# Kernel optimization log

Measured on AMD Instinct MI355X. Metric: run time of the kernel, lower is better.

The kernel has to match this reference:

```python
import jax, jax.numpy as jnp
import numpy as np

B, N, E = 4, 4096, 16384
D, A_DIM = 256, 64
T, HALF, STEPS, NTYPES = 16, 8, 3, 50


def setup_inputs() -> dict:
    key = jax.random.key(0)
    ks = jax.random.split(key, 16)
    s = 0.02  # small init so repeated DxD matmuls stay stable over 3 steps
    return {
        "annotation_id": jax.random.randint(ks[0], (B, N), 0, NTYPES),
        "src": jax.random.randint(ks[1], (B, E), 0, N),
        "dst": jax.random.randint(ks[2], (B, E), 0, N),
        "etype": jax.random.randint(ks[3], (B, E), 0, HALF),
        "edge_embed": jax.random.normal(ks[4], (T, D * D), jnp.float32) * s,
        "edge_bias": jax.random.normal(ks[5], (T, D), jnp.float32) * s,
        "type_embed": jax.random.normal(ks[6], (NTYPES, A_DIM), jnp.float32) * s,
        "Wr": jax.random.normal(ks[7], (D, 3 * D), jnp.float32) * s,
        "br": jnp.zeros((D,), jnp.float32),
        "Wz": jax.random.normal(ks[8], (D, 3 * D), jnp.float32) * s,
        "bz": jnp.zeros((D,), jnp.float32),
        "Wh": jax.random.normal(ks[9], (D, 3 * D), jnp.float32) * s,
        "bh": jnp.zeros((D,), jnp.float32),
        "Wa": jax.random.normal(ks[10], (1, D + A_DIM), jnp.float32) * s,
        "ba": jnp.zeros((1,), jnp.float32),
        "Wo": jax.random.normal(ks[11], (1, D + A_DIM), jnp.float32) * s,
        "bo": jnp.zeros((1,), jnp.float32),
    }


def reference(annotation_id, src, dst, etype, edge_embed, edge_bias, type_embed,
              Wr, br, Wz, bz, Wh, bh, Wa, ba, Wo, bo):
    # annotation: typeEmbed[id-1] if id>0 else zeros  -> [B, N, A_DIM]
    ann = jnp.where((annotation_id > 0)[..., None],
                    type_embed[jnp.clip(annotation_id - 1, 0, NTYPES - 1)],
                    jnp.zeros((), type_embed.dtype))
    # prop_state: annotation zero-padded to state_dim  -> [B, N, D]
    h = jnp.concatenate([ann, jnp.zeros((B, N, D - A_DIM), ann.dtype)], axis=-1)
    W = edge_embed.reshape(T, D, D)  # per-edge-type DxD matrices

    def step(h):
        # type-major projection: apply every edge-type matrix to every node state
        # P[b, t, n, :] = W[t] @ h[b, n]   -> [B, T, N, D]
        P = jnp.einsum('tij,bnj->btni', W, h)

        def per_graph(Pg, s_, d_, e_):
            # a_out[j]        += W[e] @ h[neighbour] + b[e]
            # a_in[neighbour] += W[e+HALF] @ h[j]   + b[e+HALF]
            m_out = Pg[e_, d_] + edge_bias[e_]            # [E, D]
            m_in = Pg[e_ + HALF, s_] + edge_bias[e_ + HALF]
            a_out = jnp.zeros((N, D), h.dtype).at[s_].add(m_out)
            a_in = jnp.zeros((N, D), h.dtype).at[d_].add(m_in)
            return a_in, a_out

        a_in, a_out = jax.vmap(per_graph)(P, src, dst, etype)
        # GRU-style propagator (dropout_rate = 0 -> identity)
        a = jnp.concatenate([a_in, a_out, h], axis=-1)    # [B, N, 3D]
        r = jax.nn.sigmoid(a @ Wr.T + br)
        z = jax.nn.sigmoid(a @ Wz.T + bz)
        h_hat = jnp.tanh(jnp.concatenate([a_in, a_out, r * h], axis=-1) @ Wh.T + bh)
        return (1.0 - z) * h + z * h_hat

    for _ in range(STEPS):
        h = step(h)

    join = jnp.concatenate([h, ann], axis=-1)             # [B, N, D+A]
    atten = jax.nn.sigmoid(join @ Wa.T + ba)              # [B, N, 1]
    ou = jnp.tanh(join @ Wo.T + bo)                       # [B, N, 1]
    w_sum = jnp.sum((atten * ou).reshape(-1, N), axis=1)  # [B]
    return jax.nn.sigmoid(w_sum)
```

## Files before the change

kernel.cpp:

```cpp
#include <hip/hip_runtime.h>
#include <cstdint>

#define BB 4
#define NN 4096
#define EE 16384
#define DD 256
#define ADIM 64
#define TT 16
#define HALFE 8
#define STEPS 3
#define OSTRIDE 4160
#define MAXTILES 1088
#define MAXM (MAXTILES * 128)

#define AS1 __attribute__((address_space(1)))
#define AS3 __attribute__((address_space(3)))

typedef __attribute__((ext_vector_type(8))) short short8;
typedef __attribute__((ext_vector_type(4))) float f32x4;

__device__ __forceinline__ float sigmoidf_(float x) { return 1.0f / (1.0f + __expf(-x)); }

__device__ __forceinline__ unsigned short f2bf(float x) {
    unsigned u = __float_as_uint(x);
    u += 0x7fffu + ((u >> 16) & 1u);
    return (unsigned short)(u >> 16);
}
__device__ __forceinline__ float bf2f(unsigned short b) {
    return __uint_as_float(((unsigned)b) << 16);
}

__global__ void init_kernel(const int* __restrict__ ann_id,
                            const float* __restrict__ type_embed,
                            float* __restrict__ ann, float* __restrict__ h,
                            unsigned short* __restrict__ hbf,
                            unsigned short* __restrict__ Xbf) {
    int idx = blockIdx.x * 256 + threadIdx.x;
    int bn = idx >> 6, q = idx & 63;
    int id = ann_id[bn];
    float4 v = {0.f, 0.f, 0.f, 0.f};
    if (q < 16) {
        if (id > 0) v = ((const float4*)(type_embed + (size_t)(id - 1) * ADIM))[q];
        ((float4*)(ann + (size_t)bn * ADIM))[q] = v;
    }
    ((float4*)(h + (size_t)bn * DD))[q] = v;
    ushort4 o;
    o.x = f2bf(v.x); o.y = f2bf(v.y); o.z = f2bf(v.z); o.w = f2bf(v.w);
    ((ushort4*)(hbf + (size_t)bn * DD))[q] = o;
    ((ushort4*)(Xbf + (size_t)bn * 768 + 512))[q] = o;
}

__global__ void conv_f2b4(const float* __restrict__ in, unsigned short* __restrict__ out) {
    int idx = blockIdx.x * 256 + threadIdx.x;
    float4 v = ((const float4*)in)[idx];
    ushort4 o;
    o.x = f2bf(v.x); o.y = f2bf(v.y); o.z = f2bf(v.z); o.w = f2bf(v.w);
    ((ushort4*)out)[idx] = o;
}

__global__ void build_wcat(const float* __restrict__ Wr, const float* __restrict__ Wz,
                           const float* __restrict__ Wh, unsigned short* __restrict__ W) {
    int idx = blockIdx.x * 256 + threadIdx.x;
    int c = idx / 768, k = idx % 768;
    float v;
    if (c < 256)       v = Wr[c * 768 + k];
    else if (c < 512)  v = Wz[(c - 256) * 768 + k];
    else               v = (k < 512) ? Wh[(c - 512) * 768 + k] : 0.f;
    W[idx] = f2bf(v);
}

__global__ void build_whh(const float* __restrict__ Wh, unsigned short* __restrict__ W) {
    int idx = blockIdx.x * 256 + threadIdx.x;
    int i = idx / 256, k = idx % 256;
    W[idx] = f2bf(Wh[i * 768 + 512 + k]);
}

__global__ void count_kernel(const int* __restrict__ src, const int* __restrict__ dst,
                             int* __restrict__ counts) {
    int idx = blockIdx.x * 256 + threadIdx.x;
    int b = idx >> 14;
    atomicAdd(&counts[(b * 2 + 0) * NN + src[idx]], 1);
    atomicAdd(&counts[(b * 2 + 1) * NN + dst[idx]], 1);
}

__global__ __launch_bounds__(1024) void scan_kernel(const int* __restrict__ counts,
                                                    int* __restrict__ offs,
                                                    int* __restrict__ cursor) {
    __shared__ int lsum[1024];
    int t = threadIdx.x, seg = blockIdx.x;
    int4 v = ((const int4*)(counts + (size_t)seg * NN))[t];
    int s1 = v.x + v.y, s2 = s1 + v.z, s3 = s2 + v.w;
    lsum[t] = s3;
    __syncthreads();
    for (int off = 1; off < 1024; off <<= 1) {
        int tmp = (t >= off) ? lsum[t - off] : 0;
        __syncthreads();
        lsum[t] += tmp;
        __syncthreads();
    }
    int base = lsum[t] - s3;
    int* o = offs + (size_t)seg * OSTRIDE;
    o[4 * t] = base; o[4 * t + 1] = base + v.x; o[4 * t + 2] = base + s1; o[4 * t + 3] = base + s2;
    if (t == 1023) o[4096] = lsum[1023];
    int* c = cursor + (size_t)seg * NN;
    c[4 * t] = base; c[4 * t + 1] = base + v.x; c[4 * t + 2] = base + s1; c[4 * t + 3] = base + s2;
}

__global__ void count2_kernel(const int* __restrict__ et, int* __restrict__ c32) {
    __shared__ int cnt[32];
    int tid = threadIdx.x;
    if (tid < 32) cnt[tid] = 0;
    __syncthreads();
    int idx = blockIdx.x * 256 + tid;
    int b = idx >> 14;
    atomicAdd(&cnt[b * 8 + et[idx]], 1);
    __syncthreads();
    if (tid < 32) atomicAdd(&c32[tid], cnt[tid]);
}

__global__ void scan2_kernel(const int* __restrict__ c32, int* __restrict__ type_cursor,
                             int* __restrict__ tile_type) {
    __shared__ int pad[64];
    int t = threadIdx.x;
    int b = t >> 4, dir = (t >> 3) & 1, tt = t & 7;
    int cnt = c32[b * 8 + tt];
    int padded = ((cnt + 127) >> 7) << 7;
    pad[t] = padded;
    __syncthreads();
    int off = 0;
    for (int k = 0; k < t; ++k) off += pad[k];
    type_cursor[t] = off;
    int t16 = dir * 8 + tt;
    int tile0 = off >> 7;
    for (int k = 0; k < (padded >> 7); ++k) tile_type[tile0 + k] = t16;
}

__global__ void fill2_kernel(const int* __restrict__ src, const int* __restrict__ dst,
                             const int* __restrict__ et, int* __restrict__ type_cursor,
                             int* __restrict__ node_cursor, int* __restrict__ entries,
                             int* __restrict__ idx2) {
    __shared__ int cnt[64];
    __shared__ int bse[64];
    int tid = threadIdx.x;
    if (tid < 64) cnt[tid] = 0;
    __syncthreads();
    int idx = blockIdx.x * 256 + tid;
    int b = idx >> 14;
    int s = src[idx], d = dst[idx], t = et[idx];
    int bin0 = b * 16 + t;
    int bin1 = b * 16 + 8 + t;
    int r0 = atomicAdd(&cnt[bin0], 1);
    int r1 = atomicAdd(&cnt[bin1], 1);
    __syncthreads();
    if (tid < 64) bse[tid] = atomicAdd(&type_cursor[tid], cnt[tid]);
    __syncthreads();
    int p0 = bse[bin0] + r0;
    int p1 = bse[bin1] + r1;
    idx2[p0] = b * NN + d;
    idx2[p1] = b * NN + s;
    int q0 = atomicAdd(&node_cursor[(b * 2 + 0) * NN + s], 1);
    entries[(size_t)(b * 2 + 0) * EE + q0] = (p0 << 4) | t;
    int q1 = atomicAdd(&node_cursor[(b * 2 + 1) * NN + d], 1);
    entries[(size_t)(b * 2 + 1) * EE + q1] = (p1 << 4) | (t + 8);
}


#define GEMM_CORE_128x64(A_, Bt_, K_)                                                   \
    const int tid = threadIdx.x;                                                        \
    const int wv = tid >> 6, lane = tid & 63;                                           \
    const int wr = wv >> 1, wc = wv & 1;                                                \
    const int lr = lane & 15, hi = lane >> 4, rx = lane & 7;                            \
    const int srow = wv * 8 + (lane >> 3);                                              \
    const int scol = ((lane & 7) ^ (lane >> 3)) << 3;                                   \
    const unsigned short* Ag = A_ + (size_t)(r0 + srow) * K_ + scol;                    \
    const unsigned short* Bg = Bt_ + (size_t)(c0 + srow) * K_ + scol;                   \
    f32x4 acc[4][2] = {};                                                               \
    for (int k0 = 0; k0 < K_; k0 += 64) {                                               \
        _Pragma("unroll")                                                               \
        for (int i = 0; i < 4; ++i)                                                     \
            __builtin_amdgcn_global_load_lds(                                           \
                (const AS1 void*)(Ag + (size_t)(i * 32) * K_ + k0),                     \
                (AS3 void*)((char*)As + wv * 1024 + i * 4096), 16, 0, 0);               \
        _Pragma("unroll")                                                               \
        for (int i = 0; i < 2; ++i)                                                     \
            __builtin_amdgcn_global_load_lds(                                           \
                (const AS1 void*)(Bg + (size_t)(i * 32) * K_ + k0),                     \
                (AS3 void*)((char*)Bs + wv * 1024 + i * 4096), 16, 0, 0);               \
        __syncthreads();                                                                \
        _Pragma("unroll")                                                               \
        for (int kk = 0; kk < 2; ++kk) {                                                \
            short8 af[4], bfv[2];                                                       \
            _Pragma("unroll")                                                           \
            for (int m = 0; m < 4; ++m) {                                               \
                int R = wr * 64 + m * 16 + lr;                                          \
                af[m] = *(const short8*)((const char*)As + R * 128 + (((kk * 4 + hi) ^ rx) << 4)); \
            }                                                                           \
            _Pragma("unroll")                                                           \
            for (int n = 0; n < 2; ++n) {                                               \
                int R = wc * 32 + n * 16 + lr;                                          \
                bfv[n] = *(const short8*)((const char*)Bs + R * 128 + (((kk * 4 + hi) ^ rx) << 4)); \
            }                                                                           \
            _Pragma("unroll")                                                           \
            for (int m = 0; m < 4; ++m)                                                 \
                _Pragma("unroll")                                                       \
                for (int n = 0; n < 2; ++n)                                             \
                    acc[m][n] = __builtin_amdgcn_mfma_f32_16x16x32_bf16(bfv[n], af[m], acc[m][n], 0, 0, 0); \
        }                                                                               \
        __syncthreads();                                                                \
    }                                                                                   \
    const int erow = r0 + wr * 64 + lr;                                                 \
    const int ecol = c0 + wc * 32 + (hi << 2);

__global__ __launch_bounds__(256) void gemm_msgs(const unsigned short* __restrict__ A,
                                                 const unsigned short* __restrict__ W2,
                                                 const int* __restrict__ idx2,
                                                 const int* __restrict__ tile_type,
                                                 unsigned short* __restrict__ C) {
    __shared__ __align__(16) unsigned short As[128 * 64];
    __shared__ __align__(16) unsigned short Bs[64 * 64];
    const int bid = blockIdx.x;
    const int wg = (bid & 7) * (MAXTILES * 4 / 8) + (bid >> 3);
    const int by = wg >> 2, bx = wg & 3;
    const int t16 = tile_type[by];
    if (t16 < 0) return;
    const int r0 = by << 7, c0 = bx << 6;
    const int tid = threadIdx.x;
    const int wv = tid >> 6, lane = tid & 63;
    const int wr = wv >> 1, wc = wv & 1;
    const int lr = lane & 15, hi = lane >> 4, rx = lane & 7;
    const int srow = wv * 8 + (lane >> 3);
    const int scol = ((lane & 7) ^ (lane >> 3)) << 3;
    int ar[4];
#pragma unroll
    for (int i = 0; i < 4; ++i) ar[i] = idx2[r0 + srow + i * 32];
    const unsigned short* Bg = W2 + (size_t)t16 * (DD * DD) + (size_t)(c0 + srow) * DD + scol;
    f32x4 acc[4][2] = {};
    for (int k0 = 0; k0 < DD; k0 += 64) {
#pragma unroll
        for (int i = 0; i < 4; ++i)
            __builtin_amdgcn_global_load_lds(
                (const AS1 void*)(A + (size_t)ar[i] * DD + scol + k0),
                (AS3 void*)((char*)As + wv * 1024 + i * 4096), 16, 0, 0);
#pragma unroll
        for (int i = 0; i < 2; ++i)
            __builtin_amdgcn_global_load_lds(
                (const AS1 void*)(Bg + (size_t)(i * 32) * DD + k0),
                (AS3 void*)((char*)Bs + wv * 1024 + i * 4096), 16, 0, 0);
        __syncthreads();
#pragma unroll
        for (int kk = 0; kk < 2; ++kk) {
            short8 af[4], bfv[2];
#pragma unroll
            for (int m = 0; m < 4; ++m) {
                int R = wr * 64 + m * 16 + lr;
                af[m] = *(const short8*)((const char*)As + R * 128 + (((kk * 4 + hi) ^ rx) << 4));
            }
#pragma unroll
            for (int n = 0; n < 2; ++n) {
                int R = wc * 32 + n * 16 + lr;
                bfv[n] = *(const short8*)((const char*)Bs + R * 128 + (((kk * 4 + hi) ^ rx) << 4));
            }
#pragma unroll
            for (int m = 0; m < 4; ++m)
#pragma unroll
                for (int n = 0; n < 2; ++n)
                    acc[m][n] = __builtin_amdgcn_mfma_f32_16x16x32_bf16(bfv[n], af[m], acc[m][n], 0, 0, 0);
        }
        __syncthreads();
    }
    const int erow = r0 + wr * 64 + lr;
    const int ecol = c0 + wc * 32 + (hi << 2);
#pragma unroll
    for (int m = 0; m < 4; ++m)
#pragma unroll
        for (int n = 0; n < 2; ++n) {
            ushort4 o;
            o.x = f2bf(acc[m][n][0]); o.y = f2bf(acc[m][n][1]);
            o.z = f2bf(acc[m][n][2]); o.w = f2bf(acc[m][n][3]);
            *(ushort4*)&C[(size_t)(erow + m * 16) * DD + ecol + n * 16] = o;
        }
}

__global__ __launch_bounds__(256) void gemm_rzu(const unsigned short* __restrict__ A,
                                                const unsigned short* __restrict__ Bt,
                                                const float* __restrict__ br,
                                                const float* __restrict__ bz,
                                                const float* __restrict__ h,
                                                unsigned short* __restrict__ RH,
                                                unsigned short* __restrict__ Zb,
                                                unsigned short* __restrict__ Ub) {
    __shared__ __align__(16) unsigned short As[128 * 64];
    __shared__ __align__(16) unsigned short Bs[64 * 64];
    const int bid = blockIdx.x;
    const int wg = (bid & 7) * 192 + (bid >> 3);
    const int bx = wg % 12, by = wg / 12;
    const int r0 = by << 7, c0 = bx << 6;
    GEMM_CORE_128x64(A, Bt, 768)
    const int region = c0 >> 8;
#pragma unroll
    for (int m = 0; m < 4; ++m)
#pragma unroll
        for (int n = 0; n < 2; ++n) {
            int gr = erow + m * 16;
            int gc = ecol + n * 16;
            f32x4 v = acc[m][n];
            if (region == 0) {
                float4 bb = *(const float4*)&br[gc];
                float4 hv = *(const float4*)&h[(size_t)gr * 256 + gc];
                ushort4 o;
                o.x = f2bf(sigmoidf_(v[0] + bb.x) * hv.x);
                o.y = f2bf(sigmoidf_(v[1] + bb.y) * hv.y);
                o.z = f2bf(sigmoidf_(v[2] + bb.z) * hv.z);
                o.w = f2bf(sigmoidf_(v[3] + bb.w) * hv.w);
                *(ushort4*)&RH[(size_t)gr * 256 + gc] = o;
            } else if (region == 1) {
                int c = gc - 256;
                float4 bb = *(const float4*)&bz[c];
                ushort4 o;
                o.x = f2bf(sigmoidf_(v[0] + bb.x));
                o.y = f2bf(sigmoidf_(v[1] + bb.y));
                o.z = f2bf(sigmoidf_(v[2] + bb.z));
                o.w = f2bf(sigmoidf_(v[3] + bb.w));
                *(ushort4*)&Zb[(size_t)gr * 256 + c] = o;
            } else {
                int c = gc - 512;
                ushort4 o;
                o.x = f2bf(v[0]); o.y = f2bf(v[1]); o.z = f2bf(v[2]); o.w = f2bf(v[3]);
                *(ushort4*)&Ub[(size_t)gr * 256 + c] = o;
            }
        }
}

__global__ __launch_bounds__(256) void gemm_hh(const unsigned short* __restrict__ A,
                                               const unsigned short* __restrict__ Bt,
                                               const unsigned short* __restrict__ Zb,
                                               const unsigned short* __restrict__ Ub,
                                               const float* __restrict__ bh,
                                               float* __restrict__ h,
                                               unsigned short* __restrict__ hbf,
                                               unsigned short* __restrict__ Xbf) {
    __shared__ __align__(16) unsigned short As[64 * 64];
    __shared__ __align__(16) unsigned short Bs[64 * 64];
    const int bid = blockIdx.x;
    const int wg = (bid & 7) * 128 + (bid >> 3);
    const int by = wg >> 2, bx = wg & 3;
    const int r0 = by << 6, c0 = bx << 6;
    const int tid = threadIdx.x;
    const int wv = tid >> 6, lane = tid & 63;
    const int wr = wv >> 1, wc = wv & 1;
    const int lr = lane & 15, hi = lane >> 4, rx = lane & 7;
    const int srow = wv * 8 + (lane >> 3);
    const int scol = ((lane & 7) ^ (lane >> 3)) << 3;
    const unsigned short* Ag = A + (size_t)(r0 + srow) * 256 + scol;
    const unsigned short* Bg = Bt + (size_t)(c0 + srow) * 256 + scol;
    f32x4 acc[2][2] = {};
    for (int k0 = 0; k0 < 256; k0 += 64) {
#pragma unroll
        for (int i = 0; i < 2; ++i) {
            __builtin_amdgcn_global_load_lds(
                (const AS1 void*)(Ag + (size_t)(i * 32) * 256 + k0),
                (AS3 void*)((char*)As + wv * 1024 + i * 4096), 16, 0, 0);
            __builtin_amdgcn_global_load_lds(
                (const AS1 void*)(Bg + (size_t)(i * 32) * 256 + k0),
                (AS3 void*)((char*)Bs + wv * 1024 + i * 4096), 16, 0, 0);
        }
        __syncthreads();
#pragma unroll
        for (int kk = 0; kk < 2; ++kk) {
            short8 af[2], bfv[2];
#pragma unroll
            for (int m = 0; m < 2; ++m) {
                int R = wr * 32 + m * 16 + lr;
                af[m] = *(const short8*)((const char*)As + R * 128 + (((kk * 4 + hi) ^ rx) << 4));
            }
#pragma unroll
            for (int n = 0; n < 2; ++n) {
                int R = wc * 32 + n * 16 + lr;
                bfv[n] = *(const short8*)((const char*)Bs + R * 128 + (((kk * 4 + hi) ^ rx) << 4));
            }
#pragma unroll
            for (int m = 0; m < 2; ++m)
#pragma unroll
                for (int n = 0; n < 2; ++n)
                    acc[m][n] = __builtin_amdgcn_mfma_f32_16x16x32_bf16(bfv[n], af[m], acc[m][n], 0, 0, 0);
        }
        __syncthreads();
    }
    const int erow = r0 + wr * 32 + lr;
    const int ecol = c0 + wc * 32 + (hi << 2);
#pragma unroll
    for (int m = 0; m < 2; ++m)
#pragma unroll
        for (int n = 0; n < 2; ++n) {
            int gr = erow + m * 16;
            int gc = ecol + n * 16;
            size_t base = (size_t)gr * 256 + gc;
            f32x4 v = acc[m][n];
            float4 bb = *(const float4*)&bh[gc];
            float4 hv = *(const float4*)&h[base];
            ushort4 zp = *(const ushort4*)&Zb[base];
            ushort4 up = *(const ushort4*)&Ub[base];
            float4 hn;
            {
                float z = bf2f(zp.x); hn.x = (1.f - z) * hv.x + z * tanhf(bf2f(up.x) + v[0] + bb.x);
            }{
                float z = bf2f(zp.y); hn.y = (1.f - z) * hv.y + z * tanhf(bf2f(up.y) + v[1] + bb.y);
            }{
                float z = bf2f(zp.z); hn.z = (1.f - z) * hv.z + z * tanhf(bf2f(up.z) + v[2] + bb.z);
            }{
                float z = bf2f(zp.w); hn.w = (1.f - z) * hv.w + z * tanhf(bf2f(up.w) + v[3] + bb.w);
            }
            *(float4*)&h[base] = hn;
            ushort4 o;
            o.x = f2bf(hn.x); o.y = f2bf(hn.y); o.z = f2bf(hn.z); o.w = f2bf(hn.w);
            *(ushort4*)&hbf[base] = o;
            *(ushort4*)&Xbf[(size_t)gr * 768 + 512 + gc] = o;
        }
}

__global__ void gather2_kernel(const unsigned short* __restrict__ msgs,
                               const int* __restrict__ offs, const int* __restrict__ entries,
                               const float* __restrict__ bias, unsigned short* __restrict__ Xb) {
    int wv = threadIdx.x >> 6, lane = threadIdx.x & 63;
    int slot = blockIdx.x * 4 + wv;
    int b = slot >> 13;
    int dir = (slot >> 12) & 1;
    int node = slot & 4095;
    const int* o = offs + (size_t)(b * 2 + dir) * OSTRIDE;
    int beg = o[node], end = o[node + 1];
    const int* ent = entries + (size_t)(b * 2 + dir) * EE;
    const float4* bias4 = (const float4*)bias;
    float4 acc = {0.f, 0.f, 0.f, 0.f};
    for (int p = beg; p < end; ++p) {
        int e2 = ent[p];
        int row = e2 >> 4, t = e2 & 15;
        ushort4 pv = *(const ushort4*)(msgs + (size_t)row * DD + lane * 4);
        float4 bv = bias4[t * 64 + lane];
        acc.x += bf2f(pv.x) + bv.x;
        acc.y += bf2f(pv.y) + bv.y;
        acc.z += bf2f(pv.z) + bv.z;
        acc.w += bf2f(pv.w) + bv.w;
    }
    ushort4 o4;
    o4.x = f2bf(acc.x); o4.y = f2bf(acc.y); o4.z = f2bf(acc.z); o4.w = f2bf(acc.w);
    int colbase = (dir == 0 ? 256 : 0) + lane * 4;
    *(ushort4*)(Xb + ((size_t)b * NN + node) * 768 + colbase) = o4;
}

__global__ void final_reduce(const float* __restrict__ h, const float* __restrict__ ann,
                             const float* __restrict__ Wa, const float* __restrict__ ba,
                             const float* __restrict__ Wo, const float* __restrict__ bo,
                             float* __restrict__ acc) {
    int wv = threadIdx.x >> 6, lane = threadIdx.x & 63;
    int b = blockIdx.x >> 5;
    int nbase = (blockIdx.x & 31) * 128 + wv * 32;
    float4 wah = ((const float4*)Wa)[lane];
    float4 woh = ((const float4*)Wo)[lane];
    float4 waa = {0, 0, 0, 0}, woa = {0, 0, 0, 0};
    if (lane < 16) {
        waa = ((const float4*)(Wa + 256))[lane];
        woa = ((const float4*)(Wo + 256))[lane];
    }
    float bav = ba[0], bov = bo[0];
    float part = 0.f;
    for (int it = 0; it < 32; ++it) {
        int node = nbase + it;
        float4 hv = ((const float4*)(h + ((size_t)b * NN + node) * DD))[lane];
        float sa = hv.x * wah.x + hv.y * wah.y + hv.z * wah.z + hv.w * wah.w;
        float so = hv.x * woh.x + hv.y * woh.y + hv.z * woh.z + hv.w * woh.w;
        if (lane < 16) {
            float4 av = ((const float4*)(ann + ((size_t)b * NN + node) * ADIM))[lane];
            sa += av.x * waa.x + av.y * waa.y + av.z * waa.z + av.w * waa.w;
            so += av.x * woa.x + av.y * woa.y + av.z * woa.z + av.w * woa.w;
        }
        for (int off = 32; off; off >>= 1) {
            sa += __shfl_down(sa, off);
            so += __shfl_down(so, off);
        }
        if (lane == 0) part += sigmoidf_(sa + bav) * tanhf(so + bov);
    }
    if (lane == 0) atomicAdd(&acc[b], part);
}

__global__ void final_out(const float* __restrict__ acc, float* __restrict__ out) {
    int b = threadIdx.x;
    if (b < BB) out[b] = sigmoidf_(acc[b]);
}

extern "C" void kernel_launch(void* const* d_in, const int* in_sizes, int n_in,
                              void* d_out, int out_size, void* d_ws, size_t ws_size,
                              hipStream_t stream) {
    const int*   ann_id     = (const int*)d_in[0];
    const int*   src        = (const int*)d_in[1];
    const int*   dst        = (const int*)d_in[2];
    const int*   etype      = (const int*)d_in[3];
    const float* edge_embed = (const float*)d_in[4];
    const float* edge_bias  = (const float*)d_in[5];
    const float* type_embed = (const float*)d_in[6];
    const float* Wr = (const float*)d_in[7];
    const float* br = (const float*)d_in[8];
    const float* Wz = (const float*)d_in[9];
    const float* bz = (const float*)d_in[10];
    const float* Wh = (const float*)d_in[11];
    const float* bh = (const float*)d_in[12];
    const float* Wa = (const float*)d_in[13];
    const float* ba = (const float*)d_in[14];
    const float* Wo = (const float*)d_in[15];
    const float* bo = (const float*)d_in[16];
    float* out = (float*)d_out;

    char* base = (char*)d_ws;
    size_t off = 0;
    auto alloc = [&](size_t bytes) { char* p = base + off; off += (bytes + 255) & ~(size_t)255; return p; };
    float* ann  = (float*)alloc((size_t)BB * NN * ADIM * 4);
    float* h    = (float*)alloc((size_t)BB * NN * DD * 4);
    float* acc  = (float*)alloc(64);
    unsigned short* h_bf   = (unsigned short*)alloc((size_t)BB * NN * DD * 2);
    unsigned short* W2bf   = (unsigned short*)alloc((size_t)TT * DD * DD * 2);
    unsigned short* Wcatbf = (unsigned short*)alloc(768 * 768 * 2);
    unsigned short* Whhbf  = (unsigned short*)alloc(256 * 256 * 2);
    unsigned short* msgs   = (unsigned short*)alloc((size_t)MAXM * DD * 2);
    unsigned short* Xbf    = (unsigned short*)alloc((size_t)BB * NN * 768 * 2);
    unsigned short* RHbf   = (unsigned short*)alloc((size_t)BB * NN * DD * 2);
    unsigned short* Zb     = (unsigned short*)alloc((size_t)BB * NN * DD * 2);
    unsigned short* Ub     = (unsigned short*)alloc((size_t)BB * NN * DD * 2);
    int* counts  = (int*)alloc((size_t)BB * 2 * NN * 4);
    int* cursor  = (int*)alloc((size_t)BB * 2 * NN * 4);
    int* offsets = (int*)alloc((size_t)BB * 2 * OSTRIDE * 4);
    int* entries = (int*)alloc((size_t)BB * 2 * EE * 4);
    int* c32     = (int*)alloc(32 * 4);
    int* tcur    = (int*)alloc(64 * 4);
    int* ttype   = (int*)alloc(MAXTILES * 4);
    int* idx2    = (int*)alloc((size_t)MAXM * 4);

    init_kernel<<<dim3((BB * NN * 64) / 256), dim3(256), 0, stream>>>(
        ann_id, type_embed, ann, h, h_bf, Xbf);
    conv_f2b4<<<dim3((TT * DD * DD) / 1024), dim3(256), 0, stream>>>(edge_embed, W2bf);
    build_wcat<<<dim3((768 * 768) / 256), dim3(256), 0, stream>>>(Wr, Wz, Wh, Wcatbf);
    build_whh<<<dim3((256 * 256) / 256), dim3(256), 0, stream>>>(Wh, Whhbf);
    hipMemsetAsync(counts, 0, (size_t)BB * 2 * NN * 4, stream);
    hipMemsetAsync(c32, 0, 32 * 4, stream);
    hipMemsetAsync(ttype, 0xFF, MAXTILES * 4, stream);
    hipMemsetAsync(idx2, 0, (size_t)MAXM * 4, stream);
    count_kernel<<<dim3((BB * EE) / 256), dim3(256), 0, stream>>>(src, dst, counts);
    count2_kernel<<<dim3((BB * EE) / 256), dim3(256), 0, stream>>>(etype, c32);
    scan_kernel<<<dim3(BB * 2), dim3(1024), 0, stream>>>(counts, offsets, cursor);
    scan2_kernel<<<dim3(1), dim3(64), 0, stream>>>(c32, tcur, ttype);
    fill2_kernel<<<dim3((BB * EE) / 256), dim3(256), 0, stream>>>(
        src, dst, etype, tcur, cursor, entries, idx2);

    for (int s = 0; s < STEPS; ++s) {
        gemm_msgs<<<dim3(MAXTILES * 4), dim3(256), 0, stream>>>(
            h_bf, W2bf, idx2, ttype, msgs);
        gather2_kernel<<<dim3(BB * 2 * NN / 4), dim3(256), 0, stream>>>(
            msgs, offsets, entries, edge_bias, Xbf);
        gemm_rzu<<<dim3(1536), dim3(256), 0, stream>>>(
            Xbf, Wcatbf, br, bz, h, RHbf, Zb, Ub);
        gemm_hh<<<dim3(1024), dim3(256), 0, stream>>>(
            RHbf, Whhbf, Zb, Ub, bh, h, h_bf, Xbf);
    }

    hipMemsetAsync(acc, 0, 64, stream);
    final_reduce<<<dim3(128), dim3(256), 0, stream>>>(h, ann, Wa, ba, Wo, bo, acc);
    final_out<<<dim3(1), dim3(64), 0, stream>>>(acc, out);
}
```

Measured before the change: 425.7 us.

## Double-buffer GEMM LDS loads and merge preprocessing kernels and memsets

Each of the three GEMM kernels now double-buffers its LDS tiles. The next K-slice is issued with global_load_lds before computing on the current one, using vmcnt waits and raw barriers in place of two __syncthreads per iteration. The goal is to overlap global-to-LDS latency with MFMA work. Separately, the four weight and state conversion kernels become one prep kernel, and the two count kernels are merged. Three memsets are absorbed into kernels or into a single larger memset, which cuts launch overhead at the cost of doubled LDS use per block, and that may lower occupancy.

Result: faster. 410.8 us (-3.5%).

```diff
diff --git a/kernel.cpp b/kernel.cpp
--- a/kernel.cpp
+++ b/kernel.cpp
@@ -30,57 +30,64 @@
     return __uint_as_float(((unsigned)b) << 16);
 }
 
-__global__ void init_kernel(const int* __restrict__ ann_id,
-                            const float* __restrict__ type_embed,
+__global__ void prep_kernel(const int* __restrict__ ann_id, const float* __restrict__ type_embed,
+                            const float* __restrict__ edge_embed, const float* __restrict__ Wr,
+                            const float* __restrict__ Wz, const float* __restrict__ Wh,
                             float* __restrict__ ann, float* __restrict__ h,
-                            unsigned short* __restrict__ hbf,
-                            unsigned short* __restrict__ Xbf) {
-    int idx = blockIdx.x * 256 + threadIdx.x;
-    int bn = idx >> 6, q = idx & 63;
-    int id = ann_id[bn];
-    float4 v = {0.f, 0.f, 0.f, 0.f};
-    if (q < 16) {
-        if (id > 0) v = ((const float4*)(type_embed + (size_t)(id - 1) * ADIM))[q];
-        ((float4*)(ann + (size_t)bn * ADIM))[q] = v;
-    }
-    ((float4*)(h + (size_t)bn * DD))[q] = v;
-    ushort4 o;
-    o.x = f2bf(v.x); o.y = f2bf(v.y); o.z = f2bf(v.z); o.w = f2bf(v.w);
-    ((ushort4*)(hbf + (size_t)bn * DD))[q] = o;
-    ((ushort4*)(Xbf + (size_t)bn * 768 + 512))[q] = o;
-}
-
-__global__ void conv_f2b4(const float* __restrict__ in, unsigned short* __restrict__ out) {
-    int idx = blockIdx.x * 256 + threadIdx.x;
-    float4 v = ((const float4*)in)[idx];
-    ushort4 o;
-    o.x = f2bf(v.x); o.y = f2bf(v.y); o.z = f2bf(v.z); o.w = f2bf(v.w);
-    ((ushort4*)out)[idx] = o;
-}
-
-__global__ void build_wcat(const float* __restrict__ Wr, const float* __restrict__ Wz,
-                           const float* __restrict__ Wh, unsigned short* __restrict__ W) {
-    int idx = blockIdx.x * 256 + threadIdx.x;
-    int c = idx / 768, k = idx % 768;
-    float v;
-    if (c < 256)       v = Wr[c * 768 + k];
-    else if (c < 512)  v = Wz[(c - 256) * 768 + k];
-    else               v = (k < 512) ? Wh[(c - 512) * 768 + k] : 0.f;
-    W[idx] = f2bf(v);
-}
-
-__global__ void build_whh(const float* __restrict__ Wh, unsigned short* __restrict__ W) {
-    int idx = blockIdx.x * 256 + threadIdx.x;
-    int i = idx / 256, k = idx % 256;
-    W[idx] = f2bf(Wh[i * 768 + 512 + k]);
-}
-
-__global__ void count_kernel(const int* __restrict__ src, const int* __restrict__ dst,
-                             int* __restrict__ counts) {
-    int idx = blockIdx.x * 256 + threadIdx.x;
+                            unsigned short* __restrict__ hbf, unsigned short* __restrict__ Xbf,
+                            unsigned short* __restrict__ W2bf, unsigned short* __restrict__ Wcatbf,
+                            unsigned short* __restrict__ Whhbf, float* __restrict__ acc) {
+    int bid = blockIdx.x, tid = threadIdx.x;
+    if (bid < 4096) {
+        if (bid == 0 && tid < 16) acc[tid] = 0.f;
+        int idx = bid * 256 + tid;
+        int bn = idx >> 6, q = idx & 63;
+        int id = ann_id[bn];
+        float4 v = {0.f, 0.f, 0.f, 0.f};
+        if (q < 16) {
+            if (id > 0) v = ((const float4*)(type_embed + (size_t)(id - 1) * ADIM))[q];
+            ((float4*)(ann + (size_t)bn * ADIM))[q] = v;
+        }
+        ((float4*)(h + (size_t)bn * DD))[q] = v;
+        ushort4 o;
+        o.x = f2bf(v.x); o.y = f2bf(v.y); o.z = f2bf(v.z); o.w = f2bf(v.w);
+        ((ushort4*)(hbf + (size_t)bn * DD))[q] = o;
+        ((ushort4*)(Xbf + (size_t)bn * 768 + 512))[q] = o;
+    } else if (bid < 5120) {
+        int idx = (bid - 4096) * 256 + tid;
+        float4 v = ((const float4*)edge_embed)[idx];
+        ushort4 o;
+        o.x = f2bf(v.x); o.y = f2bf(v.y); o.z = f2bf(v.z); o.w = f2bf(v.w);
+        ((ushort4*)W2bf)[idx] = o;
+    } else if (bid < 7424) {
+        int idx = (bid - 5120) * 256 + tid;
+        int c = idx / 768, k = idx % 768;
+        float v;
+        if (c < 256)       v = Wr[c * 768 + k];
+        else if (c < 512)  v = Wz[(c - 256) * 768 + k];
+        else               v = (k < 512) ? Wh[(c - 512) * 768 + k] : 0.f;
+        Wcatbf[idx] = f2bf(v);
+    } else {
+        int idx = (bid - 7424) * 256 + tid;
+        int i = idx / 256, k = idx % 256;
+        Whhbf[idx] = f2bf(Wh[i * 768 + 512 + k]);
+    }
+}
+
+__global__ void count_all(const int* __restrict__ src, const int* __restrict__ dst,
+                          const int* __restrict__ et, int* __restrict__ counts,
+                          int* __restrict__ c32) {
+    __shared__ int cnt[32];
+    int tid = threadIdx.x;
+    if (tid < 32) cnt[tid] = 0;
+    __syncthreads();
+    int idx = blockIdx.x * 256 + tid;
     int b = idx >> 14;
     atomicAdd(&counts[(b * 2 + 0) * NN + src[idx]], 1);
     atomicAdd(&counts[(b * 2 + 1) * NN + dst[idx]], 1);
+    atomicAdd(&cnt[b * 8 + et[idx]], 1);
+    __syncthreads();
+    if (tid < 32) atomicAdd(&c32[tid], cnt[tid]);
 }
 
 __global__ __launch_bounds__(1024) void scan_kernel(const int* __restrict__ counts,
@@ -106,22 +113,12 @@
     c[4 * t] = base; c[4 * t + 1] = base + v.x; c[4 * t + 2] = base + s1; c[4 * t + 3] = base + s2;
 }
 
-__global__ void count2_kernel(const int* __restrict__ et, int* __restrict__ c32) {
-    __shared__ int cnt[32];
-    int tid = threadIdx.x;
-    if (tid < 32) cnt[tid] = 0;
-    __syncthreads();
-    int idx = blockIdx.x * 256 + tid;
-    int b = idx >> 14;
-    atomicAdd(&cnt[b * 8 + et[idx]], 1);
-    __syncthreads();
-    if (tid < 32) atomicAdd(&c32[tid], cnt[tid]);
-}
-
 __global__ void scan2_kernel(const int* __restrict__ c32, int* __restrict__ type_cursor,
-                             int* __restrict__ tile_type) {
+                             int* __restrict__ tile_type, int* __restrict__ idx2) {
     __shared__ int pad[64];
     int t = threadIdx.x;
+    for (int k = t; k < MAXTILES; k += 64) tile_type[k] = -1;
+    __syncthreads();
     int b = t >> 4, dir = (t >> 3) & 1, tt = t & 7;
     int cnt = c32[b * 8 + tt];
     int padded = ((cnt + 127) >> 7) << 7;
@@ -133,6 +130,7 @@
     int t16 = dir * 8 + tt;
     int tile0 = off >> 7;
     for (int k = 0; k < (padded >> 7); ++k) tile_type[tile0 + k] = t16;
+    for (int r = off + cnt; r < off + padded; ++r) idx2[r] = 0;
 }
 
 __global__ void fill2_kernel(const int* __restrict__ src, const int* __restrict__ dst,
@@ -165,59 +163,39 @@
 }
 
 
-#define GEMM_CORE_128x64(A_, Bt_, K_)                                                   \
-    const int tid = threadIdx.x;                                                        \
-    const int wv = tid >> 6, lane = tid & 63;                                           \
-    const int wr = wv >> 1, wc = wv & 1;                                                \
-    const int lr = lane & 15, hi = lane >> 4, rx = lane & 7;                            \
-    const int srow = wv * 8 + (lane >> 3);                                              \
-    const int scol = ((lane & 7) ^ (lane >> 3)) << 3;                                   \
-    const unsigned short* Ag = A_ + (size_t)(r0 + srow) * K_ + scol;                    \
-    const unsigned short* Bg = Bt_ + (size_t)(c0 + srow) * K_ + scol;                   \
-    f32x4 acc[4][2] = {};                                                               \
-    for (int k0 = 0; k0 < K_; k0 += 64) {                                               \
+#define COMP_128x64(cb)                                                                 \
+    _Pragma("unroll")                                                                   \
+    for (int kk = 0; kk < 2; ++kk) {                                                    \
+        short8 af[4], bfv[2];                                                           \
         _Pragma("unroll")                                                               \
-        for (int i = 0; i < 4; ++i)                                                     \
-            __builtin_amdgcn_global_load_lds(                                           \
-                (const AS1 void*)(Ag + (size_t)(i * 32) * K_ + k0),                     \
-                (AS3 void*)((char*)As + wv * 1024 + i * 4096), 16, 0, 0);               \
+        for (int m = 0; m < 4; ++m) {                                                   \
+            int R = wr * 64 + m * 16 + lr;                                              \
+            af[m] = *(const short8*)((const char*)As + (cb) * 16384 + R * 128 + (((kk * 4 + hi) ^ rx) << 4)); \
+        }                                                                               \
         _Pragma("unroll")                                                               \
-        for (int i = 0; i < 2; ++i)                                                     \
-            __builtin_amdgcn_global_load_lds(                                           \
-                (const AS1 void*)(Bg + (size_t)(i * 32) * K_ + k0),                     \
-                (AS3 void*)((char*)Bs + wv * 1024 + i * 4096), 16, 0, 0);               \
-        __syncthreads();                                                                \
+        for (int n = 0; n < 2; ++n) {                                                   \
+            int R = wc * 32 + n * 16 + lr;                                              \
+            bfv[n] = *(const short8*)((const char*)Bs + (cb) * 8192 + R * 128 + (((kk * 4 + hi) ^ rx) << 4)); \
+        }                                                                               \
         _Pragma("unroll")                                                               \
-        for (int kk = 0; kk < 2; ++kk) {                                                \
-            short8 af[4], bfv[2];                                                       \
+        for (int m = 0; m < 4; ++m)                                                     \
             _Pragma("unroll")                                                           \
-            for (int m = 0; m < 4; ++m) {                                               \
-                int R = wr * 64 + m * 16 + lr;                                          \
-                af[m] = *(const short8*)((const char*)As + R * 128 + (((kk * 4 + hi) ^ rx) << 4)); \
-            }                                                                           \
-            _Pragma("unroll")                                                           \
-            for (int n = 0; n < 2; ++n) {                                               \
-                int R = wc * 32 + n * 16 + lr;                                          \
-                bfv[n] = *(const short8*)((const char*)Bs + R * 128 + (((kk * 4 + hi) ^ rx) << 4)); \
-            }                                                                           \
-            _Pragma("unroll")                                                           \
-            for (int m = 0; m < 4; ++m)                                                 \
-                _Pragma("unroll")                                                       \
-                for (int n = 0; n < 2; ++n)                                             \
-                    acc[m][n] = __builtin_amdgcn_mfma_f32_16x16x32_bf16(bfv[n], af[m], acc[m][n], 0, 0, 0); \
-        }                                                                               \
-        __syncthreads();                                                                \
-    }                                                                                   \
-    const int erow = r0 + wr * 64 + lr;                                                 \
-    const int ecol = c0 + wc * 32 + (hi << 2);
+            for (int n = 0; n < 2; ++n)                                                 \
+                acc[m][n] = __builtin_amdgcn_mfma_f32_16x16x32_bf16(bfv[n], af[m], acc[m][n], 0, 0, 0); \
+    }
+
+#define PIPE_WAIT(NSTR)                                                                 \
+    asm volatile("s_waitcnt vmcnt(" NSTR ")" ::: "memory");                             \
+    __builtin_amdgcn_s_barrier();                                                       \
+    __builtin_amdgcn_sched_barrier(0);
 
 __global__ __launch_bounds__(256) void gemm_msgs(const unsigned short* __restrict__ A,
                                                  const unsigned short* __restrict__ W2,
                                                  const int* __restrict__ idx2,
                                                  const int* __restrict__ tile_type,
                                                  unsigned short* __restrict__ C) {
-    __shared__ __align__(16) unsigned short As[128 * 64];
-    __shared__ __align__(16) unsigned short Bs[64 * 64];
+    __shared__ __align__(16) unsigned short As[2 * 128 * 64];
+    __shared__ __align__(16) unsigned short Bs[2 * 64 * 64];
     const int bid = blockIdx.x;
     const int wg = (bid & 7) * (MAXTILES * 4 / 8) + (bid >> 3);
     const int by = wg >> 2, bx = wg & 3;
@@ -235,39 +213,26 @@
     for (int i = 0; i < 4; ++i) ar[i] = idx2[r0 + srow + i * 32];
     const unsigned short* Bg = W2 + (size_t)t16 * (DD * DD) + (size_t)(c0 + srow) * DD + scol;
     f32x4 acc[4][2] = {};
-    for (int k0 = 0; k0 < DD; k0 += 64) {
-#pragma unroll
-        for (int i = 0; i < 4; ++i)
-            __builtin_amdgcn_global_load_lds(
-                (const AS1 void*)(A + (size_t)ar[i] * DD + scol + k0),
-                (AS3 void*)((char*)As + wv * 1024 + i * 4096), 16, 0, 0);
-#pragma unroll
-        for (int i = 0; i < 2; ++i)
-            __builtin_amdgcn_global_load_lds(
-                (const AS1 void*)(Bg + (size_t)(i * 32) * DD + k0),
-                (AS3 void*)((char*)Bs + wv * 1024 + i * 4096), 16, 0, 0);
-        __syncthreads();
-#pragma unroll
-        for (int kk = 0; kk < 2; ++kk) {
-            short8 af[4], bfv[2];
-#pragma unroll
-            for (int m = 0; m < 4; ++m) {
-                int R = wr * 64 + m * 16 + lr;
-                af[m] = *(const short8*)((const char*)As + R * 128 + (((kk * 4 + hi) ^ rx) << 4));
-            }
-#pragma unroll
-            for (int n = 0; n < 2; ++n) {
-                int R = wc * 32 + n * 16 + lr;
-                bfv[n] = *(const short8*)((const char*)Bs + R * 128 + (((kk * 4 + hi) ^ rx) << 4));
-            }
-#pragma unroll
-            for (int m = 0; m < 4; ++m)
-#pragma unroll
-                for (int n = 0; n < 2; ++n)
-                    acc[m][n] = __builtin_amdgcn_mfma_f32_16x16x32_bf16(bfv[n], af[m], acc[m][n], 0, 0, 0);
-        }
-        __syncthreads();
-    }
+#define MS_STG(buf, kof)                                                                \
+    { _Pragma("unroll")                                                                 \
+      for (int i = 0; i < 4; ++i)                                                       \
+          __builtin_amdgcn_global_load_lds(                                             \
+              (const AS1 void*)(A + (size_t)ar[i] * DD + scol + (kof)),                 \
+              (AS3 void*)((char*)As + (buf) * 16384 + wv * 1024 + i * 4096), 16, 0, 0); \
+      _Pragma("unroll")                                                                 \
+      for (int i = 0; i < 2; ++i)                                                       \
+          __builtin_amdgcn_global_load_lds(                                             \
+              (const AS1 void*)(Bg + (size_t)(i * 32) * DD + (kof)),                    \
+              (AS3 void*)((char*)Bs + (buf) * 8192 + wv * 1024 + i * 4096), 16, 0, 0); }
+    MS_STG(0, 0)
+    for (int it = 0; it < 3; ++it) {
+        MS_STG((it + 1) & 1, (it + 1) * 64)
+        PIPE_WAIT("6")
+        COMP_128x64(it & 1)
+        __builtin_amdgcn_s_barrier();
+    }
+    PIPE_WAIT("0")
+    COMP_128x64(1)
     const int erow = r0 + wr * 64 + lr;
     const int ecol = c0 + wc * 32 + (hi << 2);
 #pragma unroll
@@ -289,13 +254,43 @@
                                                 unsigned short* __restrict__ RH,
                                                 unsigned short* __restrict__ Zb,
                                                 unsigned short* __restrict__ Ub) {
-    __shared__ __align__(16) unsigned short As[128 * 64];
-    __shared__ __align__(16) unsigned short Bs[64 * 64];
+    __shared__ __align__(16) unsigned short As[2 * 128 * 64];
+    __shared__ __align__(16) unsigned short Bs[2 * 64 * 64];
     const int bid = blockIdx.x;
     const int wg = (bid & 7) * 192 + (bid >> 3);
     const int bx = wg % 12, by = wg / 12;
     const int r0 = by << 7, c0 = bx << 6;
-    GEMM_CORE_128x64(A, Bt, 768)
+    const int tid = threadIdx.x;
+    const int wv = tid >> 6, lane = tid & 63;
+    const int wr = wv >> 1, wc = wv & 1;
+    const int lr = lane & 15, hi = lane >> 4, rx = lane & 7;
+    const int srow = wv * 8 + (lane >> 3);
+    const int scol = ((lane & 7) ^ (lane >> 3)) << 3;
+    const unsigned short* Ag = A + (size_t)(r0 + srow) * 768 + scol;
+    const unsigned short* Bg = Bt + (size_t)(c0 + srow) * 768 + scol;
+    f32x4 acc[4][2] = {};
+#define RZ_STG(buf, kof)                                                                \
+    { _Pragma("unroll")                                                                 \
+      for (int i = 0; i < 4; ++i)                                                       \
+          __builtin_amdgcn_global_load_lds(                                             \
+              (const AS1 void*)(Ag + (size_t)(i * 32) * 768 + (kof)),                   \
+              (AS3 void*)((char*)As + (buf) * 16384 + wv * 1024 + i * 4096), 16, 0, 0); \
+      _Pragma("unroll")                                                                 \
+      for (int i = 0; i < 2; ++i)                                                       \
+          __builtin_amdgcn_global_load_lds(                                             \
+              (const AS1 void*)(Bg + (size_t)(i * 32) * 768 + (kof)),                   \
+              (AS3 void*)((char*)Bs + (buf) * 8192 + wv * 1024 + i * 4096), 16, 0, 0); }
+    RZ_STG(0, 0)
+    for (int it = 0; it < 11; ++it) {
+        RZ_STG((it + 1) & 1, (it + 1) * 64)
+        PIPE_WAIT("6")
+        COMP_128x64(it & 1)
+        __builtin_amdgcn_s_barrier();
+    }
+    PIPE_WAIT("0")
+    COMP_128x64(1)
+    const int erow = r0 + wr * 64 + lr;
+    const int ecol = c0 + wc * 32 + (hi << 2);
     const int region = c0 >> 8;
 #pragma unroll
     for (int m = 0; m < 4; ++m)
@@ -339,8 +334,8 @@
                                                float* __restrict__ h,
                                                unsigned short* __restrict__ hbf,
                                                unsigned short* __restrict__ Xbf) {
-    __shared__ __align__(16) unsigned short As[64 * 64];
-    __shared__ __align__(16) unsigned short Bs[64 * 64];
+    __shared__ __align__(16) unsigned short As[2 * 64 * 64];
+    __shared__ __align__(16) unsigned short Bs[2 * 64 * 64];
     const int bid = blockIdx.x;
     const int wg = (bid & 7) * 128 + (bid >> 3);
     const int by = wg >> 2, bx = wg & 3;
@@ -354,38 +349,44 @@
     const unsigned short* Ag = A + (size_t)(r0 + srow) * 256 + scol;
     const unsigned short* Bg = Bt + (size_t)(c0 + srow) * 256 + scol;
     f32x4 acc[2][2] = {};
-    for (int k0 = 0; k0 < 256; k0 += 64) {
-#pragma unroll
-        for (int i = 0; i < 2; ++i) {
-            __builtin_amdgcn_global_load_lds(
-                (const AS1 void*)(Ag + (size_t)(i * 32) * 256 + k0),
-                (AS3 void*)((char*)As + wv * 1024 + i * 4096), 16, 0, 0);
-            __builtin_amdgcn_global_load_lds(
-                (const AS1 void*)(Bg + (size_t)(i * 32) * 256 + k0),
-                (AS3 void*)((char*)Bs + wv * 1024 + i * 4096), 16, 0, 0);
-        }
-        __syncthreads();
-#pragma unroll
-        for (int kk = 0; kk < 2; ++kk) {
-            short8 af[2], bfv[2];
-#pragma unroll
-            for (int m = 0; m < 2; ++m) {
-                int R = wr * 32 + m * 16 + lr;
-                af[m] = *(const short8*)((const char*)As + R * 128 + (((kk * 4 + hi) ^ rx) << 4));
-            }
-#pragma unroll
-            for (int n = 0; n < 2; ++n) {
-                int R = wc * 32 + n * 16 + lr;
-                bfv[n] = *(const short8*)((const char*)Bs + R * 128 + (((kk * 4 + hi) ^ rx) << 4));
-            }
-#pragma unroll
-            for (int m = 0; m < 2; ++m)
-#pragma unroll
-                for (int n = 0; n < 2; ++n)
-                    acc[m][n] = __builtin_amdgcn_mfma_f32_16x16x32_bf16(bfv[n], af[m], acc[m][n], 0, 0, 0);
-        }
-        __syncthreads();
-    }
+#define HH_STG(buf, kof)                                                                \
+    { _Pragma("unroll")                                                                 \
+      for (int i = 0; i < 2; ++i) {                                                     \
+          __builtin_amdgcn_global_load_lds(                                             \
+              (const AS1 void*)(Ag + (size_t)(i * 32) * 256 + (kof)),                   \
+              (AS3 void*)((char*)As + (buf) * 8192 + wv * 1024 + i * 4096), 16, 0, 0);  \
+          __builtin_amdgcn_global_load_lds(                                             \
+              (const AS1 void*)(Bg + (size_t)(i * 32) * 256 + (kof)),                   \
+              (AS3 void*)((char*)Bs + (buf) * 8192 + wv * 1024 + i * 4096), 16, 0, 0); } }
+#define COMP_64x64(cb)                                                                  \
+    _Pragma("unroll")                                                                   \
+    for (int kk = 0; kk < 2; ++kk) {                                                    \
+        short8 af[2], bfv[2];                                                           \
+        _Pragma("unroll")                                                               \
+        for (int m = 0; m < 2; ++m) {                                                   \
+            int R = wr * 32 + m * 16 + lr;                                              \
+            af[m] = *(const short8*)((const char*)As + (cb) * 8192 + R * 128 + (((kk * 4 + hi) ^ rx) << 4)); \
+        }                                                                               \
+        _Pragma("unroll")                                                               \
+        for (int n = 0; n < 2; ++n) {                                                   \
+            int R = wc * 32 + n * 16 + lr;                                              \
+            bfv[n] = *(const short8*)((const char*)Bs + (cb) * 8192 + R * 128 + (((kk * 4 + hi) ^ rx) << 4)); \
+        }                                                                               \
+        _Pragma("unroll")                                                               \
+        for (int m = 0; m < 2; ++m)                                                     \
+            _Pragma("unroll")                                                           \
+            for (int n = 0; n < 2; ++n)                                                 \
+                acc[m][n] = __builtin_amdgcn_mfma_f32_16x16x32_bf16(bfv[n], af[m], acc[m][n], 0, 0, 0); \
+    }
+    HH_STG(0, 0)
+    for (int it = 0; it < 3; ++it) {
+        HH_STG((it + 1) & 1, (it + 1) * 64)
+        PIPE_WAIT("4")
+        COMP_64x64(it & 1)
+        __builtin_amdgcn_s_barrier();
+    }
+    PIPE_WAIT("0")
+    COMP_64x64(1)
     const int erow = r0 + wr * 32 + lr;
     const int ecol = c0 + wc * 32 + (hi << 2);
 #pragma unroll
@@ -525,27 +526,21 @@
     unsigned short* Zb     = (unsigned short*)alloc((size_t)BB * NN * DD * 2);
     unsigned short* Ub     = (unsigned short*)alloc((size_t)BB * NN * DD * 2);
     int* counts  = (int*)alloc((size_t)BB * 2 * NN * 4);
+    int* c32     = (int*)alloc(32 * 4);
     int* cursor  = (int*)alloc((size_t)BB * 2 * NN * 4);
     int* offsets = (int*)alloc((size_t)BB * 2 * OSTRIDE * 4);
     int* entries = (int*)alloc((size_t)BB * 2 * EE * 4);
-    int* c32     = (int*)alloc(32 * 4);
     int* tcur    = (int*)alloc(64 * 4);
     int* ttype   = (int*)alloc(MAXTILES * 4);
     int* idx2    = (int*)alloc((size_t)MAXM * 4);
 
-    init_kernel<<<dim3((BB * NN * 64) / 256), dim3(256), 0, stream>>>(
-        ann_id, type_embed, ann, h, h_bf, Xbf);
-    conv_f2b4<<<dim3((TT * DD * DD) / 1024), dim3(256), 0, stream>>>(edge_embed, W2bf);
-    build_wcat<<<dim3((768 * 768) / 256), dim3(256), 0, stream>>>(Wr, Wz, Wh, Wcatbf);
-    build_whh<<<dim3((256 * 256) / 256), dim3(256), 0, stream>>>(Wh, Whhbf);
-    hipMemsetAsync(counts, 0, (size_t)BB * 2 * NN * 4, stream);
-    hipMemsetAsync(c32, 0, 32 * 4, stream);
-    hipMemsetAsync(ttype, 0xFF, MAXTILES * 4, stream);
-    hipMemsetAsync(idx2, 0, (size_t)MAXM * 4, stream);
-    count_kernel<<<dim3((BB * EE) / 256), dim3(256), 0, stream>>>(src, dst, counts);
-    count2_kernel<<<dim3((BB * EE) / 256), dim3(256), 0, stream>>>(etype, c32);
+    prep_kernel<<<dim3(7680), dim3(256), 0, stream>>>(
+        ann_id, type_embed, edge_embed, Wr, Wz, Wh,
+        ann, h, h_bf, Xbf, W2bf, Wcatbf, Whhbf, acc);
+    hipMemsetAsync(counts, 0, (size_t)BB * 2 * NN * 4 + 256, stream);
+    count_all<<<dim3((BB * EE) / 256), dim3(256), 0, stream>>>(src, dst, etype, counts, c32);
     scan_kernel<<<dim3(BB * 2), dim3(1024), 0, stream>>>(counts, offsets, cursor);
-    scan2_kernel<<<dim3(1), dim3(64), 0, stream>>>(c32, tcur, ttype);
+    scan2_kernel<<<dim3(1), dim3(64), 0, stream>>>(c32, tcur, ttype, idx2);
     fill2_kernel<<<dim3((BB * EE) / 256), dim3(256), 0, stream>>>(
         src, dst, etype, tcur, cursor, entries, idx2);
 
@@ -560,7 +555,6 @@
             RHbf, Whhbf, Zb, Ub, bh, h, h_bf, Xbf);
     }
 
-    hipMemsetAsync(acc, 0, 64, stream);
     final_reduce<<<dim3(128), dim3(256), 0, stream>>>(h, ann, Wa, ba, Wo, bo, acc);
     final_out<<<dim3(1), dim3(64), 0, stream>>>(acc, out);
 }
```
